# Performance work log

Hardware: AMD Instinct MI355X
Metric: run time of the kernel (lower is better)

The kernel has to match this reference:

```python
import jax, jax.numpy as jnp
import numpy as np

B, S, D_IN, D_OUT, P, T = 8, 1024, 1024, 1024, 128, 8  # T = emo_class_num + 1


def setup_inputs() -> dict:
    key = jax.random.key(0)
    ks = jax.random.split(key, 10)
    w = lambda k, shp, s=0.02: (jax.random.normal(k, shp, dtype=jnp.float32) * s)
    return {
        "x": jax.random.normal(ks[0], (B, S, D_IN), dtype=jnp.float32),
        "p_cla": jax.random.normal(ks[1], (B, S, P), dtype=jnp.float32),
        "W_emo": w(ks[2], (D_IN, D_OUT)),
        "b_emo": jnp.zeros((D_OUT,), jnp.float32),
        "W_att": w(ks[3], (D_OUT, D_OUT)),
        "b_att": jnp.zeros((D_OUT,), jnp.float32),
        "W_hid": w(ks[4], (P + D_OUT, T)),
        "b_hid": jnp.zeros((T,), jnp.float32),
        "crf_start": w(ks[5], (T,), 0.1),
        "crf_end": w(ks[6], (T,), 0.1),
        "crf_trans": w(ks[7], (T, T), 0.1),
        "emo_list": jax.random.randint(ks[8], (B, S), 0, T),
    }


def _crf_nll(em, tags, start, end, trans):
    # em: [B,S,T] emissions; tags: [B,S] int. Negative log-likelihood (sum over batch).
    num = (start[tags[:, 0]]
           + jnp.take_along_axis(em, tags[..., None], axis=2)[..., 0].sum(axis=1)
           + trans[tags[:, :-1], tags[:, 1:]].sum(axis=1)
           + end[tags[:, -1]])  # [B]
    alpha0 = start[None, :] + em[:, 0]  # [B,T]

    def step(alpha, e_t):
        # alpha: [B,T], e_t: [B,T]
        a = jax.nn.logsumexp(alpha[:, :, None] + trans[None, :, :] + e_t[:, None, :], axis=1)
        return a, None

    alpha, _ = jax.lax.scan(step, alpha0, jnp.swapaxes(em, 0, 1)[1:])
    logZ = jax.nn.logsumexp(alpha + end[None, :], axis=-1)  # [B]
    return jnp.sum(logZ - num)


def reference(x, p_cla, W_emo, b_emo, W_att, b_att, W_hid, b_hid,
              crf_start, crf_end, crf_trans, emo_list):
    out = jax.nn.relu(x @ W_emo + b_emo)                 # [B,S,D]
    out_att = out @ W_att + b_att                        # [B,S,D]
    att = jax.nn.softmax(jnp.einsum('bsd,btd->bst', out_att, out), axis=-1)
    out = jnp.einsum('bst,btd->bsd', att, out)           # [B,S,D]
    z_dec = jnp.concatenate([p_cla, out], axis=-1)       # [B,S,P+D]
    em = z_dec @ W_hid + b_hid                           # [B,S,T]
    return _crf_nll(em, emo_list, crf_start, crf_end, crf_trans)
```

## Files before the change

kernel.cpp:

```cpp
#include <hip/hip_runtime.h>
#include <stdint.h>

typedef unsigned short u16;
typedef __attribute__((ext_vector_type(8))) short bf16x8;
typedef __attribute__((ext_vector_type(4))) float f32x4;

#define NB 8
#define SEQ 1024
#define DDIM 1024
#define NP 128
#define NT 8
#define GK 1024
#define NKT 16

__device__ __forceinline__ u16 f2b(float f){
  union { float f; uint32_t u; } v; v.f = f;
  return (u16)((v.u + 0x7FFFu + ((v.u >> 16) & 1u)) >> 16);
}
__device__ __forceinline__ float b2f(u16 h){
  union { uint32_t u; float f; } v; v.u = ((uint32_t)h) << 16; return v.f;
}

__device__ __forceinline__ void load_lds16(const void* g, void* l){
  __builtin_amdgcn_global_load_lds((const __attribute__((address_space(1))) void*)g,
                                   (__attribute__((address_space(3))) void*)l,
                                   16, 0, 0);
}

#define MEMFENCE asm volatile("" ::: "memory")
#define SBAR() do { MEMFENCE; __builtin_amdgcn_s_barrier(); MEMFENCE; } while(0)

__global__ __launch_bounds__(256) void prep_kernel(const float* __restrict__ x,
                                                   u16* __restrict__ xb,
                                                   const float* __restrict__ W0,
                                                   const float* __restrict__ W1,
                                                   u16* __restrict__ T0,
                                                   u16* __restrict__ T1,
                                                   float* __restrict__ rowsum,
                                                   float* __restrict__ dout){
  __shared__ float tile[32][33];
  const int bid = blockIdx.x;
  const int tid = threadIdx.x;
  if(bid < 8192){
    int idx = (bid * 256 + tid) * 4;
    float4 v = *(const float4*)(x + idx);
    ushort4 o;
    o.x = f2b(v.x); o.y = f2b(v.y); o.z = f2b(v.z); o.w = f2b(v.w);
    *(ushort4*)(xb + idx) = o;
  } else {
    const int b2 = bid - 8192;
    const int z  = b2 >> 10;
    const int bx = b2 & 31, by = (b2 >> 5) & 31;
    const int tx = tid & 31, ty = tid >> 5;
    const float* W = z ? W1 : W0;
    u16* Wt = z ? T1 : T0;
    const int c0 = bx * 32, r0 = by * 32;
    for(int i = ty; i < 32; i += 8)
      tile[i][tx] = W[(size_t)(r0 + i) * DDIM + c0 + tx];
    __syncthreads();
    for(int i = ty; i < 32; i += 8)
      Wt[(size_t)(c0 + i) * DDIM + r0 + tx] = f2b(tile[tx][i]);
    if(z == 0 && by == 0)
      rowsum[bx * 256 + tid] = 0.f;
    if(b2 == 0 && tid == 0)
      dout[0] = 0.f;
  }
}

template<int MODE, bool RELU>
__global__ __launch_bounds__(512, 2) void gemm_bt(
    const u16* __restrict__ A, const u16* __restrict__ Bt,
    const float* __restrict__ bias, float* __restrict__ rowsum,
    u16* __restrict__ Cv,
    int gm, int N, long long bA, long long bB, long long bC)
{
  __shared__ u16 As[3][256][64];
  __shared__ u16 Bs[3][128][64];

  const int tid  = threadIdx.x;
  const int lane = tid & 63;
  const int wid  = tid >> 6;
  const int wr   = wid >> 1;
  const int wc   = wid & 1;

  int id = blockIdx.x;
  const int chunk = gridDim.x >> 3;
  id = (id & 7) * chunk + (id >> 3);
  const int tn = id & 7;
  const int tm = (id >> 3) % gm;
  const int bz = (id >> 3) / gm;

  const char* gAp = (const char*)(A  + (size_t)bz * bA + (size_t)tm * 256 * GK);
  const char* gBp = (const char*)(Bt + (size_t)bz * bB + (size_t)tn * 128 * GK);
  const int colg = ((tid & 7) * 16) ^ (((tid >> 3) & 7) << 4);
  const char* gA0 = gAp + (size_t)(tid >> 3) * 2048 + colg;
  const char* gB0 = gBp + (size_t)(tid >> 3) * 2048 + colg;
  char* lA0 = (char*)&As[0][0][0] + tid * 16;
  char* lB0 = (char*)&Bs[0][0][0] + tid * 16;
  const int SLA = 256 * 64 * 2;
  const int SLB = 128 * 64 * 2;

  auto stageA = [&](int slot, int tt){
    const int g = tt * 128;
#pragma unroll
    for(int q = 0; q < 4; q++)
      load_lds16(gA0 + (size_t)q * 64 * 2048 + g, lA0 + slot * SLA + q * 8192);
  };
  auto stageB = [&](int slot, int tt){
    const int g = tt * 128;
#pragma unroll
    for(int q = 0; q < 2; q++)
      load_lds16(gB0 + (size_t)q * 64 * 2048 + g, lB0 + slot * SLB + q * 8192);
  };

  f32x4 acc[4][4];
#pragma unroll
  for(int i = 0; i < 4; i++)
#pragma unroll
    for(int j = 0; j < 4; j++){ acc[i][j][0]=0.f; acc[i][j][1]=0.f; acc[i][j][2]=0.f; acc[i][j][3]=0.f; }

  const int fr = lane & 15, kq = lane >> 4;
  const int a0 = (kq * 16) ^ ((fr & 7) << 4);
  const int a1 = a0 ^ 64;
  const char* aRd = (const char*)&As[0][0][0] + (wr * 64 + fr) * 128;
  const char* bRd = (const char*)&Bs[0][0][0] + (wc * 64 + fr) * 128;

  stageA(0, 0); stageB(0, 0);
  stageA(1, 1); stageB(1, 1);

  int slot = 0, slotp = 2;
  for(int t = 0; t < NKT; ++t){
    if(t < NKT - 1){ asm volatile("s_waitcnt vmcnt(6)" ::: "memory"); }
    else           { asm volatile("s_waitcnt vmcnt(0)" ::: "memory"); }
    SBAR();

    const char* ab = aRd + slot * SLA;
    const char* bb = bRd + slot * SLB;
    bf16x8 av[4], bv[4], aw[4], bw[4];
#pragma unroll
    for(int mi = 0; mi < 4; mi++) av[mi] = *(const bf16x8*)(ab + mi * 2048 + a0);
#pragma unroll
    for(int ni = 0; ni < 4; ni++) bv[ni] = *(const bf16x8*)(bb + ni * 2048 + a0);
#pragma unroll
    for(int mi = 0; mi < 4; mi++) aw[mi] = *(const bf16x8*)(ab + mi * 2048 + a1);
#pragma unroll
    for(int ni = 0; ni < 4; ni++) bw[ni] = *(const bf16x8*)(bb + ni * 2048 + a1);
    if(t + 2 < NKT){ stageA(slotp, t + 2); stageB(slotp, t + 2); }

    __builtin_amdgcn_s_setprio(1);
#pragma unroll
    for(int mi = 0; mi < 4; mi++)
#pragma unroll
      for(int ni = 0; ni < 4; ni++)
        acc[mi][ni] = __builtin_amdgcn_mfma_f32_16x16x32_bf16(av[mi], bv[ni], acc[mi][ni], 0, 0, 0);
#pragma unroll
    for(int mi = 0; mi < 4; mi++)
#pragma unroll
      for(int ni = 0; ni < 4; ni++)
        acc[mi][ni] = __builtin_amdgcn_mfma_f32_16x16x32_bf16(aw[mi], bw[ni], acc[mi][ni], 0, 0, 0);
    __builtin_amdgcn_s_setprio(0);

    slot  = (slot  == 2) ? 0 : slot  + 1;
    slotp = (slotp == 2) ? 0 : slotp + 1;
  }

  const int m0 = tm * 256 + wr * 64;
  const int n0 = tn * 128 + wc * 64;
  const int rq = lane >> 4;

  if(MODE == 0){
#pragma unroll
    for(int ni = 0; ni < 4; ni++){
      const int gcol = n0 + ni * 16 + fr;
      const float bv = bias[gcol];
#pragma unroll
      for(int mi = 0; mi < 4; mi++){
#pragma unroll
        for(int r = 0; r < 4; r++){
          const int grow = m0 + mi * 16 + rq * 4 + r;
          float v = acc[mi][ni][r] + bv;
          if(RELU) v = fmaxf(v, 0.f);
          Cv[(size_t)bz * bC + (size_t)grow * N + gcol] = f2b(v);
        }
      }
    }
  } else {
    float rs[4][4];
#pragma unroll
    for(int mi = 0; mi < 4; mi++)
#pragma unroll
      for(int r = 0; r < 4; r++) rs[mi][r] = 0.f;
#pragma unroll
    for(int ni = 0; ni < 4; ni++){
      const int gcol = n0 + ni * 16 + fr;
#pragma unroll
      for(int mi = 0; mi < 4; mi++){
#pragma unroll
        for(int r = 0; r < 4; r++){
          const int grow = m0 + mi * 16 + rq * 4 + r;
          float e = __expf(acc[mi][ni][r]);
          rs[mi][r] += e;
          Cv[(size_t)bz * bC + (size_t)grow * N + gcol] = f2b(e);
        }
      }
    }
#pragma unroll
    for(int off = 1; off < 16; off <<= 1)
#pragma unroll
      for(int mi = 0; mi < 4; mi++)
#pragma unroll
        for(int r = 0; r < 4; r++) rs[mi][r] += __shfl_xor(rs[mi][r], off);
    if(fr == 0){
#pragma unroll
      for(int mi = 0; mi < 4; mi++)
#pragma unroll
        for(int r = 0; r < 4; r++){
          const int grow = m0 + mi * 16 + rq * 4 + r;
          atomicAdd(&rowsum[bz * SEQ + grow], rs[mi][r]);
        }
    }
  }
}

__global__ __launch_bounds__(256) void vw_kernel(const u16* __restrict__ outb,
                                                 const float* __restrict__ Whid,
                                                 float* __restrict__ VW){
  const int row  = blockIdx.x * 4 + (threadIdx.x >> 6);
  const int lane = threadIdx.x & 63;
  const u16* o = outb + (size_t)row * 1024;
  float s[8] = {0.f,0.f,0.f,0.f,0.f,0.f,0.f,0.f};
#pragma unroll
  for(int h = 0; h < 16; h++){
    const int d = lane + 64 * h;
    const float od = b2f(o[d]);
    const float4 w0 = *(const float4*)(Whid + (size_t)(NP + d) * 8);
    const float4 w1 = *(const float4*)(Whid + (size_t)(NP + d) * 8 + 4);
    s[0] += od * w0.x; s[1] += od * w0.y; s[2] += od * w0.z; s[3] += od * w0.w;
    s[4] += od * w1.x; s[5] += od * w1.y; s[6] += od * w1.z; s[7] += od * w1.w;
  }
#pragma unroll
  for(int off = 1; off < 64; off <<= 1)
#pragma unroll
    for(int j = 0; j < 8; j++) s[j] += __shfl_xor(s[j], off);
  if(lane == 0){
#pragma unroll
    for(int j = 0; j < 8; j++) VW[(size_t)row * 8 + j] = s[j];
  }
}

__global__ __launch_bounds__(256) void em2_kernel(const u16* __restrict__ scores,
                                                  const float* __restrict__ pcla,
                                                  const float* __restrict__ VW,
                                                  const float* __restrict__ rowsum,
                                                  const float* __restrict__ Whid,
                                                  const float* __restrict__ bhid,
                                                  float* __restrict__ em){
  const int row  = blockIdx.x * 4 + (threadIdx.x >> 6);
  const int lane = threadIdx.x & 63;
  const int bz   = row >> 10;
  const u16* pr = scores + (size_t)row * 1024;
  const float* vwb = VW + (size_t)bz * 8192;
  float sa[8] = {0.f,0.f,0.f,0.f,0.f,0.f,0.f,0.f};
  float sp[8] = {0.f,0.f,0.f,0.f,0.f,0.f,0.f,0.f};
#pragma unroll
  for(int h = 0; h < 16; h++){
    const int t = lane + 64 * h;
    const float pv = b2f(pr[t]);
    const float4 v0 = *(const float4*)(vwb + (size_t)t * 8);
    const float4 v1 = *(const float4*)(vwb + (size_t)t * 8 + 4);
    sa[0] += pv * v0.x; sa[1] += pv * v0.y; sa[2] += pv * v0.z; sa[3] += pv * v0.w;
    sa[4] += pv * v1.x; sa[5] += pv * v1.y; sa[6] += pv * v1.z; sa[7] += pv * v1.w;
  }
#pragma unroll
  for(int q = 0; q < 2; q++){
    const int p = lane * 2 + q;
    const float pv = pcla[(size_t)row * NP + p];
    const float4 w0 = *(const float4*)(Whid + (size_t)p * 8);
    const float4 w1 = *(const float4*)(Whid + (size_t)p * 8 + 4);
    sp[0] += pv * w0.x; sp[1] += pv * w0.y; sp[2] += pv * w0.z; sp[3] += pv * w0.w;
    sp[4] += pv * w1.x; sp[5] += pv * w1.y; sp[6] += pv * w1.z; sp[7] += pv * w1.w;
  }
#pragma unroll
  for(int off = 1; off < 64; off <<= 1)
#pragma unroll
    for(int j = 0; j < 8; j++){
      sa[j] += __shfl_xor(sa[j], off);
      sp[j] += __shfl_xor(sp[j], off);
    }
  if(lane == 0){
    const float inv = 1.f / rowsum[row];
#pragma unroll
    for(int j = 0; j < 8; j++)
      em[(size_t)row * 8 + j] = sa[j] * inv + sp[j] + bhid[j];
  }
}

__global__ __launch_bounds__(256) void crf_kernel(const float* __restrict__ em,
                                                  const int* __restrict__ tags,
                                                  const float* __restrict__ cstart,
                                                  const float* __restrict__ cend,
                                                  const float* __restrict__ ctrans,
                                                  float* __restrict__ out){
  const int b = blockIdx.x;
  const int tid = threadIdx.x;
  const float* emb = em + (size_t)b * SEQ * 8;
  const int* tg = tags + b * SEQ;

  __shared__ float Mbuf[128][64];
  __shared__ float Mbuf2[64][64];
  __shared__ float ls1[128], ls2[64];
  __shared__ float etr_s[64];
  __shared__ float mxs[64];
  __shared__ float red[256];

  if(tid < 64) etr_s[tid] = expf(ctrans[tid]);

  float loc = 0.f;
  for(int t = tid; t < SEQ; t += 256){
    const int tgt = tg[t];
    loc += emb[t * 8 + tgt];
    if(t < SEQ - 1) loc += ctrans[tgt * 8 + tg[t + 1]];
  }
  if(tid == 0) loc += cstart[tg[0]] + cend[tg[SEQ - 1]];
  red[tid] = loc;
  __syncthreads();
  for(int s = 128; s > 0; s >>= 1){
    if(tid < s) red[tid] += red[tid + s];
    __syncthreads();
  }

  if(tid < 128){
    const int c = tid;
    const int t0 = (c == 0) ? 1 : c * 8;
    const int t1 = c * 8 + 8;
    float etr[64];
#pragma unroll
    for(int i = 0; i < 64; i++) etr[i] = etr_s[i];
    float acc[64];
    float ej[8];
#pragma unroll
    for(int j = 0; j < 8; j++) ej[j] = expf(emb[t0 * 8 + j]);
#pragma unroll
    for(int i = 0; i < 8; i++)
#pragma unroll
      for(int j = 0; j < 8; j++) acc[i * 8 + j] = etr[i * 8 + j] * ej[j];
    for(int t = t0 + 1; t < t1; t++){
#pragma unroll
      for(int j = 0; j < 8; j++) ej[j] = expf(emb[t * 8 + j]);
#pragma unroll
      for(int i = 0; i < 8; i++){
        float tmp[8];
#pragma unroll
        for(int j = 0; j < 8; j++){
          float sv = 0.f;
#pragma unroll
          for(int k = 0; k < 8; k++) sv += acc[i * 8 + k] * etr[k * 8 + j];
          tmp[j] = sv * ej[j];
        }
#pragma unroll
        for(int j = 0; j < 8; j++) acc[i * 8 + j] = tmp[j];
      }
    }
    float mx = acc[0];
#pragma unroll
    for(int i = 1; i < 64; i++) mx = fmaxf(mx, acc[i]);
    const float im = 1.f / mx;
#pragma unroll
    for(int i = 0; i < 64; i++) Mbuf[c][i] = acc[i] * im;
    ls1[c] = logf(mx);
  }
  __syncthreads();

  float* src = &Mbuf[0][0];  float* dst = &Mbuf2[0][0];
  float* lsrc = ls1;         float* ldst = ls2;
  for(int n = 64; n >= 1; n >>= 1){
    for(int idx = tid; idx < n * 64; idx += 256){
      const int p = idx >> 6, e = idx & 63, i = e >> 3, j = e & 7;
      const float* Am = src + (size_t)(2 * p) * 64;
      const float* Bm = src + (size_t)(2 * p + 1) * 64;
      float sv = 0.f;
#pragma unroll
      for(int k = 0; k < 8; k++) sv += Am[i * 8 + k] * Bm[k * 8 + j];
      dst[(size_t)p * 64 + e] = sv;
    }
    __syncthreads();
    if(tid < n){
      const float* Cm = dst + (size_t)tid * 64;
      float mx = Cm[0];
#pragma unroll
      for(int i = 1; i < 64; i++) mx = fmaxf(mx, Cm[i]);
      mxs[tid] = 1.f / mx;
      ldst[tid] = lsrc[2 * tid] + lsrc[2 * tid + 1] + logf(mx);
    }
    __syncthreads();
    for(int idx = tid; idx < n * 64; idx += 256)
      dst[idx] *= mxs[idx >> 6];
    __syncthreads();
    float* tf = src; src = dst; dst = tf;
    float* tl = lsrc; lsrc = ldst; ldst = tl;
  }

  if(tid == 0){
    float a0[8];
#pragma unroll
    for(int i = 0; i < 8; i++) a0[i] = expf(cstart[i] + emb[i]);
    float z = 0.f;
#pragma unroll
    for(int j = 0; j < 8; j++){
      float t = 0.f;
#pragma unroll
      for(int i = 0; i < 8; i++) t += a0[i] * src[i * 8 + j];
      z += t * expf(cend[j]);
    }
    const float logZ = logf(z) + lsrc[0];
    atomicAdd(out, logZ - red[0]);
  }
}

extern "C" void kernel_launch(void* const* d_in, const int* in_sizes, int n_in,
                              void* d_out, int out_size, void* d_ws, size_t ws_size,
                              hipStream_t stream){
  (void)in_sizes; (void)n_in; (void)out_size; (void)ws_size;
  const float* x      = (const float*)d_in[0];
  const float* p_cla  = (const float*)d_in[1];
  const float* W_emo  = (const float*)d_in[2];
  const float* b_emo  = (const float*)d_in[3];
  const float* W_att  = (const float*)d_in[4];
  const float* b_att  = (const float*)d_in[5];
  const float* W_hid  = (const float*)d_in[6];
  const float* b_hid  = (const float*)d_in[7];
  const float* cstart = (const float*)d_in[8];
  const float* cend   = (const float*)d_in[9];
  const float* ctrans = (const float*)d_in[10];
  const int*   tags   = (const int*)d_in[11];

  char* ws = (char*)d_ws;
  const size_t MB = 1u << 20;
  u16*   xb     = (u16*)(ws + 0 * MB);
  u16*   wemoT  = (u16*)(ws + 16 * MB);
  u16*   wattT  = (u16*)(ws + 18 * MB);
  u16*   out_b  = (u16*)(ws + 20 * MB);
  u16*   oatt   = (u16*)(ws + 36 * MB);
  u16*   scores = (u16*)(ws + 52 * MB);
  float* VW     = (float*)(ws + 68 * MB);
  float* em     = (float*)(ws + 69 * MB);
  float* rowsum = (float*)(ws + 70 * MB);

  const long long bs = (long long)SEQ * DDIM;

  prep_kernel<<<8192 + 2048, 256, 0, stream>>>(x, xb, W_emo, W_att, wemoT, wattT,
                                               rowsum, (float*)d_out);

  gemm_bt<0, true><<<256, 512, 0, stream>>>(
      xb, wemoT, b_emo, nullptr, out_b, 32, DDIM, 0, 0, 0);
  gemm_bt<0, false><<<256, 512, 0, stream>>>(
      out_b, wattT, b_att, nullptr, oatt, 32, DDIM, 0, 0, 0);
  gemm_bt<1, false><<<256, 512, 0, stream>>>(
      oatt, out_b, nullptr, rowsum, scores, 4, SEQ, bs, bs, bs);
  vw_kernel<<<2048, 256, 0, stream>>>(out_b, W_hid, VW);
  em2_kernel<<<2048, 256, 0, stream>>>(scores, p_cla, VW, rowsum, W_hid, b_hid, em);
  crf_kernel<<<NB, 256, 0, stream>>>(em, tags, cstart, cend, ctrans, (float*)d_out);
}
```

Baseline: 126.9 us.

## Fuse softmax-times-VW projection into scores GEMM epilogue, drop scores matrix

The scores GEMM epilogue now multiplies the exponentiated scores by the per-column VW projection (loaded into LDS) and writes per-column-tile partial 8-wide sums, so the 16 MB bf16 scores matrix is never written or re-read. vw_kernel is moved before the GEMM, and the em kernel only reduces the eight partials per row. This removes a large global write and read, in exchange for more ALU work and extra shuffles in the GEMM epilogue, which may raise register pressure.

```diff
diff --git a/kernel.cpp b/kernel.cpp
--- a/kernel.cpp
+++ b/kernel.cpp
@@ -72,10 +72,12 @@
     const u16* __restrict__ A, const u16* __restrict__ Bt,
     const float* __restrict__ bias, float* __restrict__ rowsum,
     u16* __restrict__ Cv,
-    int gm, int N, long long bA, long long bB, long long bC)
+    int gm, int N, long long bA, long long bB, long long bC,
+    const float* __restrict__ VWg, float* __restrict__ part)
 {
   __shared__ u16 As[3][256][64];
   __shared__ u16 Bs[3][128][64];
+  __shared__ float wv[MODE == 1 ? 128 : 1][9];
 
   const int tid  = threadIdx.x;
   const int lane = tid & 63;
@@ -89,6 +91,16 @@
   const int tn = id & 7;
   const int tm = (id >> 3) % gm;
   const int bz = (id >> 3) / gm;
+
+  if(MODE == 1){
+    if(tid < 256){
+      const int rr = tid >> 1, half = (tid & 1) * 4;
+      float4 vv = *(const float4*)(VWg + ((size_t)bz * SEQ + tn * 128 + rr) * 8 + half);
+      wv[rr][half + 0] = vv.x; wv[rr][half + 1] = vv.y;
+      wv[rr][half + 2] = vv.z; wv[rr][half + 3] = vv.w;
+    }
+    __syncthreads();
+  }
 
   const char* gAp = (const char*)(A  + (size_t)bz * bA + (size_t)tm * 256 * GK);
   const char* gBp = (const char*)(Bt + (size_t)bz * bB + (size_t)tn * 128 * GK);
@@ -191,16 +203,39 @@
 #pragma unroll
       for(int r = 0; r < 4; r++) rs[mi][r] = 0.f;
 #pragma unroll
-    for(int ni = 0; ni < 4; ni++){
-      const int gcol = n0 + ni * 16 + fr;
-#pragma unroll
-      for(int mi = 0; mi < 4; mi++){
+    for(int mi = 0; mi < 4; mi++){
+      float vs[4][8];
+#pragma unroll
+      for(int r = 0; r < 4; r++)
+#pragma unroll
+        for(int j = 0; j < 8; j++) vs[r][j] = 0.f;
+#pragma unroll
+      for(int ni = 0; ni < 4; ni++){
+        const int lc = wc * 64 + ni * 16 + fr;
+#pragma unroll
+        for(int r = 0; r < 4; r++){
+          const float e = __expf(acc[mi][ni][r]);
+          rs[mi][r] += e;
+#pragma unroll
+          for(int j = 0; j < 8; j++) vs[r][j] += e * wv[lc][j];
+        }
+      }
+#pragma unroll
+      for(int off = 1; off < 16; off <<= 1)
+#pragma unroll
+        for(int r = 0; r < 4; r++)
+#pragma unroll
+          for(int j = 0; j < 8; j++) vs[r][j] += __shfl_xor(vs[r][j], off);
+      if(fr == 0){
 #pragma unroll
         for(int r = 0; r < 4; r++){
           const int grow = m0 + mi * 16 + rq * 4 + r;
-          float e = __expf(acc[mi][ni][r]);
-          rs[mi][r] += e;
-          Cv[(size_t)bz * bC + (size_t)grow * N + gcol] = f2b(e);
+          float4 p0, p1;
+          p0.x = vs[r][0]; p0.y = vs[r][1]; p0.z = vs[r][2]; p0.w = vs[r][3];
+          p1.x = vs[r][4]; p1.y = vs[r][5]; p1.z = vs[r][6]; p1.w = vs[r][7];
+          float* dst = part + ((size_t)bz * SEQ + grow) * 64 + tn * 8;
+          *(float4*)dst = p0;
+          *(float4*)(dst + 4) = p1;
         }
       }
     }
@@ -248,29 +283,19 @@
   }
 }
 
-__global__ __launch_bounds__(256) void em2_kernel(const u16* __restrict__ scores,
+__global__ __launch_bounds__(256) void em3_kernel(const float* __restrict__ part,
                                                   const float* __restrict__ pcla,
-                                                  const float* __restrict__ VW,
                                                   const float* __restrict__ rowsum,
                                                   const float* __restrict__ Whid,
                                                   const float* __restrict__ bhid,
                                                   float* __restrict__ em){
   const int row  = blockIdx.x * 4 + (threadIdx.x >> 6);
   const int lane = threadIdx.x & 63;
-  const int bz   = row >> 10;
-  const u16* pr = scores + (size_t)row * 1024;
-  const float* vwb = VW + (size_t)bz * 8192;
-  float sa[8] = {0.f,0.f,0.f,0.f,0.f,0.f,0.f,0.f};
+  float sa = part[(size_t)row * 64 + lane];
+  sa += __shfl_xor(sa, 8);
+  sa += __shfl_xor(sa, 16);
+  sa += __shfl_xor(sa, 32);
   float sp[8] = {0.f,0.f,0.f,0.f,0.f,0.f,0.f,0.f};
-#pragma unroll
-  for(int h = 0; h < 16; h++){
-    const int t = lane + 64 * h;
-    const float pv = b2f(pr[t]);
-    const float4 v0 = *(const float4*)(vwb + (size_t)t * 8);
-    const float4 v1 = *(const float4*)(vwb + (size_t)t * 8 + 4);
-    sa[0] += pv * v0.x; sa[1] += pv * v0.y; sa[2] += pv * v0.z; sa[3] += pv * v0.w;
-    sa[4] += pv * v1.x; sa[5] += pv * v1.y; sa[6] += pv * v1.z; sa[7] += pv * v1.w;
-  }
 #pragma unroll
   for(int q = 0; q < 2; q++){
     const int p = lane * 2 + q;
@@ -283,15 +308,10 @@
 #pragma unroll
   for(int off = 1; off < 64; off <<= 1)
 #pragma unroll
-    for(int j = 0; j < 8; j++){
-      sa[j] += __shfl_xor(sa[j], off);
-      sp[j] += __shfl_xor(sp[j], off);
-    }
-  if(lane == 0){
+    for(int j = 0; j < 8; j++) sp[j] += __shfl_xor(sp[j], off);
+  if(lane < 8){
     const float inv = 1.f / rowsum[row];
-#pragma unroll
-    for(int j = 0; j < 8; j++)
-      em[(size_t)row * 8 + j] = sa[j] * inv + sp[j] + bhid[j];
+    em[(size_t)row * 8 + lane] = sa * inv + sp[lane] + bhid[lane];
   }
 }
 
@@ -441,10 +461,10 @@
   u16*   wattT  = (u16*)(ws + 18 * MB);
   u16*   out_b  = (u16*)(ws + 20 * MB);
   u16*   oatt   = (u16*)(ws + 36 * MB);
-  u16*   scores = (u16*)(ws + 52 * MB);
-  float* VW     = (float*)(ws + 68 * MB);
-  float* em     = (float*)(ws + 69 * MB);
-  float* rowsum = (float*)(ws + 70 * MB);
+  float* part   = (float*)(ws + 52 * MB);
+  float* VW     = (float*)(ws + 54 * MB);
+  float* em     = (float*)(ws + 55 * MB);
+  float* rowsum = (float*)(ws + 56 * MB);
 
   const long long bs = (long long)SEQ * DDIM;
 
@@ -452,12 +472,12 @@
                                                rowsum, (float*)d_out);
 
   gemm_bt<0, true><<<256, 512, 0, stream>>>(
-      xb, wemoT, b_emo, nullptr, out_b, 32, DDIM, 0, 0, 0);
+      xb, wemoT, b_emo, nullptr, out_b, 32, DDIM, 0, 0, 0, nullptr, nullptr);
   gemm_bt<0, false><<<256, 512, 0, stream>>>(
-      out_b, wattT, b_att, nullptr, oatt, 32, DDIM, 0, 0, 0);
+      out_b, wattT, b_att, nullptr, oatt, 32, DDIM, 0, 0, 0, nullptr, nullptr);
+  vw_kernel<<<2048, 256, 0, stream>>>(out_b, W_hid, VW);
   gemm_bt<1, false><<<256, 512, 0, stream>>>(
-      oatt, out_b, nullptr, rowsum, scores, 4, SEQ, bs, bs, bs);
-  vw_kernel<<<2048, 256, 0, stream>>>(out_b, W_hid, VW);
-  em2_kernel<<<2048, 256, 0, stream>>>(scores, p_cla, VW, rowsum, W_hid, b_hid, em);
+      oatt, out_b, nullptr, rowsum, nullptr, 4, SEQ, bs, bs, 0, VW, part);
+  em3_kernel<<<2048, 256, 0, stream>>>(part, p_cla, rowsum, W_hid, b_hid, em);
   crf_kernel<<<NB, 256, 0, stream>>>(em, tags, cstart, cend, ctrans, (float*)d_out);
 }
```

New measurement: 127.9 us. No clear change (+0.8%).
